# Optimization experiments

Hardware: AMD Instinct MI355X
Metric: run time of the kernel (lower is better)

## Reference

```python
import jax, jax.numpy as jnp
import numpy as np

WS = 7          # window size
NH = 12         # num heads
DIM = 384
HID = 4 * DIM
EPS = 1e-5


def _rel_pos_index(ws):
    coords = np.stack(np.meshgrid(np.arange(ws), np.arange(ws), indexing='ij'))  # (2,ws,ws)
    cf = coords.reshape(2, -1)
    rel = cf[:, :, None] - cf[:, None, :]           # (2,N,N)
    rel = rel.transpose(1, 2, 0)                    # (N,N,2)
    rel[:, :, 0] += ws - 1
    rel[:, :, 1] += ws - 1
    rel[:, :, 0] *= 2 * ws - 1
    return jnp.asarray(rel.sum(-1))                 # (N,N) int

REL_IDX = _rel_pos_index(WS)


def _layernorm(x, g, b):
    m = x.mean(-1, keepdims=True)
    v = ((x - m) ** 2).mean(-1, keepdims=True)
    return (x - m) * jax.lax.rsqrt(v + EPS) * g + b


def setup_inputs() -> dict:
    key = jax.random.key(0)
    ks = jax.random.split(key, 16)
    B, H, W = 8, 112, 112
    s = lambda fan: 1.0 / np.sqrt(fan)
    return {
        'x': jax.random.normal(ks[0], (B, DIM, H, W), jnp.float32),
        'g1': jnp.ones((DIM,), jnp.float32),
        'b1': jnp.zeros((DIM,), jnp.float32),
        'w_qkv': jax.random.normal(ks[1], (DIM, 3 * DIM), jnp.float32) * s(DIM),
        'b_qkv': jnp.zeros((3 * DIM,), jnp.float32),
        'rpb': jax.random.normal(ks[2], ((2 * WS - 1) ** 2, NH), jnp.float32) * 0.02,
        'w_proj': jax.random.normal(ks[3], (DIM, DIM), jnp.float32) * s(DIM),
        'b_proj': jnp.zeros((DIM,), jnp.float32),
        'g2': jnp.ones((DIM,), jnp.float32),
        'b2': jnp.zeros((DIM,), jnp.float32),
        'w_fc1': jax.random.normal(ks[4], (DIM, HID), jnp.float32) * s(DIM),
        'b_fc1': jnp.zeros((HID,), jnp.float32),
        'w_fc2': jax.random.normal(ks[5], (HID, DIM), jnp.float32) * s(HID),
        'b_fc2': jnp.zeros((DIM,), jnp.float32),
    }


def reference(x, g1, b1, w_qkv, b_qkv, rpb, w_proj, b_proj, g2, b2, w_fc1, b_fc1, w_fc2, b_fc2):
    B, C, H, W = x.shape
    x = x.transpose(0, 2, 3, 1)                     # (B,H,W,C)
    shortcut = x
    xn = _layernorm(x, g1, b1)

    # window partition (with padding, no-op when divisible)
    pad_h = (-H) % WS
    pad_w = (-W) % WS
    if pad_h or pad_w:
        xn = jnp.pad(xn, ((0, 0), (0, pad_h), (0, pad_w), (0, 0)))
    Hp, Wp = H + pad_h, W + pad_w
    N = WS * WS
    xw = xn.reshape(B, Hp // WS, WS, Wp // WS, WS, C).transpose(0, 1, 3, 2, 4, 5)
    xw = xw.reshape(-1, N, C)                       # (B_, N, C)
    B_ = xw.shape[0]
    hd = C // NH

    qkv = (xw @ w_qkv + b_qkv).reshape(B_, N, 3, NH, hd)
    q = qkv[:, :, 0].transpose(0, 2, 1, 3) * (hd ** -0.5)   # (B_,h,N,d)
    k = qkv[:, :, 1].transpose(0, 2, 1, 3)
    v = qkv[:, :, 2].transpose(0, 2, 1, 3)

    attn = jnp.einsum('bhnd,bhmd->bhnm', q, k)
    bias = rpb[REL_IDX.reshape(-1)].reshape(N, N, NH).transpose(2, 0, 1)  # (h,N,N)
    attn = jax.nn.softmax(attn + bias[None], axis=-1)

    out = jnp.einsum('bhnm,bhmd->bhnd', attn, v).transpose(0, 2, 1, 3).reshape(B_, N, C)
    out = out @ w_proj + b_proj

    # window reverse
    out = out.reshape(B, Hp // WS, Wp // WS, WS, WS, C).transpose(0, 1, 3, 2, 4, 5)
    out = out.reshape(B, Hp, Wp, C)[:, :H, :W]

    x = shortcut + out
    h = _layernorm(x, g2, b2)
    h = jax.nn.gelu(h @ w_fc1 + b_fc1, approximate=False) @ w_fc2 + b_fc2
    x = x + h
    return x.transpose(0, 3, 1, 2)                  # (B,C,H,W)
```

## Files before the change

kernel.cpp:

```cpp
#include <hip/hip_runtime.h>
#include <cstdint>
#include <cmath>

using u16 = unsigned short;

typedef __bf16 bf16x8 __attribute__((ext_vector_type(8)));
typedef float  f32x4  __attribute__((ext_vector_type(4)));

__device__ __forceinline__ float b2f(u16 u) {
    return __uint_as_float(((unsigned int)u) << 16);
}
__device__ __forceinline__ u16 f2b(float f) {
    unsigned int x = __float_as_uint(f);
    unsigned int r = (x + 0x7fffu + ((x >> 16) & 1u)) >> 16;
    return (u16)r;
}
__device__ __forceinline__ u16 f2b_fast(float f) {
    union { __bf16 h; u16 u; } cv;
    cv.h = (__bf16)f;
    return cv.u;
}

__device__ __forceinline__ void gload16(const u16* g, u16* l) {
    __builtin_amdgcn_global_load_lds((__attribute__((address_space(1))) void*)g,
                                     (__attribute__((address_space(3))) void*)l,
                                     16, 0, 0);
}

#define LGKM0_FENCE() do { \
    asm volatile("s_waitcnt lgkmcnt(0)" ::: "memory"); \
    __builtin_amdgcn_sched_barrier(0); } while (0)

__device__ __forceinline__ float gelu_f(float x) {
    float z = fabsf(x) * 0.70710678118f;
    float t = __builtin_amdgcn_rcpf(fmaf(0.3275911f, z, 1.0f));
    float poly = fmaf(fmaf(fmaf(fmaf(1.061405429f, t, -1.453152027f),
                               t, 1.421413741f),
                          t, -0.284496736f),
                     t, 0.254829592f) * t;
    float e = __expf(-z * z);
    float erfv = copysignf(1.0f - poly * e, x);
    return 0.5f * x * (1.0f + erfv);
}

__device__ __forceinline__ int tprime(int b, int hw) {
    int r = hw / 112, c = hw - r * 112;
    int wy = r / 7, iy = r - wy * 7;
    int wx = c / 7, ix = c - wx * 7;
    return (b * 256 + wy * 16 + wx) * 49 + iy * 7 + ix;
}

__global__ void detect_dtype(const unsigned int* __restrict__ x, int* __restrict__ flag) {
    __shared__ int cnt[256];
    int tid = threadIdx.x;
    int c = 0;
#pragma unroll
    for (int i = 0; i < 16; ++i) {
        unsigned int w = x[tid * 16 + i];
        int e = (w >> 23) & 0xFF;
        if (e >= 100 && e <= 150) ++c;
    }
    cnt[tid] = c;
    __syncthreads();
    if (tid == 0) {
        int s = 0;
        for (int i = 0; i < 256; ++i) s += cnt[i];
        flag[0] = (s > 3072) ? 1 : 0;
    }
}

__global__ void prep_small(const void* g1, const void* b1, const void* bqkv,
                           const void* bproj, const void* g2, const void* b2,
                           const void* bfc1, const void* bfc2, const void* rpb,
                           u16* cg1, u16* cb1, u16* cbqkv, u16* cbproj,
                           u16* cg2, u16* cb2, u16* cbfc1, u16* cbfc2,
                           float* bias_exp, const int* __restrict__ flagp) {
    int isf = flagp[0];
    int tid = threadIdx.x;
    auto cv = [&](const void* s, int i) {
        return isf ? f2b(((const float*)s)[i]) : ((const u16*)s)[i];
    };
    for (int i = tid; i < 384; i += 256) cg1[i] = cv(g1, i);
    for (int i = tid; i < 384; i += 256) cb1[i] = cv(b1, i);
    for (int i = tid; i < 1152; i += 256) cbqkv[i] = cv(bqkv, i);
    for (int i = tid; i < 384; i += 256) cbproj[i] = cv(bproj, i);
    for (int i = tid; i < 384; i += 256) cg2[i] = cv(g2, i);
    for (int i = tid; i < 384; i += 256) cb2[i] = cv(b2, i);
    for (int i = tid; i < 1536; i += 256) cbfc1[i] = cv(bfc1, i);
    for (int i = tid; i < 384; i += 256) cbfc2[i] = cv(bfc2, i);
    for (int i = tid; i < 12 * 64 * 64; i += 256) {
        int h = i >> 12, row = (i >> 6) & 63, col = i & 63;
        float v = -1e30f;
        if (row < 49 && col < 49) {
            int ri = row / 7, rj = row - ri * 7;
            int mi = col / 7, mj = col - mi * 7;
            int idx = ((ri - mi + 6) * 13 + (rj - mj + 6)) * 12 + h;
            v = isf ? ((const float*)rpb)[idx] : b2f(((const u16*)rpb)[idx]);
        }
        bias_exp[i] = v;
    }
}

__global__ void prep_w(const void* w0, const void* w1, const void* w2, const void* w3,
                       u16* o0, u16* o1, u16* o2, u16* o3,
                       const int* __restrict__ flagp) {
    __shared__ u16 tile[32][33];
    int isf = flagp[0];
    const void* src; u16* dst; int K, N;
    switch (blockIdx.z) {
        case 0: src = w0; dst = o0; K = 384;  N = 1152; break;
        case 1: src = w1; dst = o1; K = 384;  N = 384;  break;
        case 2: src = w2; dst = o2; K = 384;  N = 1536; break;
        default: src = w3; dst = o3; K = 1536; N = 384; break;
    }
    if ((int)blockIdx.x >= N / 32 || (int)blockIdx.y >= K / 32) return;
    int n0 = blockIdx.x * 32, k0 = blockIdx.y * 32;
    int tx = threadIdx.x & 31, ty = threadIdx.x >> 5;
#pragma unroll
    for (int i = 0; i < 4; ++i) {
        size_t idx = (size_t)(k0 + ty + i * 8) * N + n0 + tx;
        tile[ty + i * 8][tx] = isf ? f2b(((const float*)src)[idx])
                                   : ((const u16*)src)[idx];
    }
    __syncthreads();
#pragma unroll
    for (int i = 0; i < 4; ++i)
        dst[(size_t)(n0 + ty + i * 8) * K + k0 + tx] = tile[tx][ty + i * 8];
}

__global__ void ln1_fused(const void* __restrict__ x, const u16* __restrict__ g1,
                          const u16* __restrict__ b1, u16* __restrict__ xt,
                          u16* __restrict__ xn, const int* __restrict__ flagp) {
    __shared__ float tile[64][66];
    __shared__ float part[4][64];
    __shared__ float part2[4][64];
    __shared__ float stat[2][64];
    int isf = flagp[0];
    int hw0 = blockIdx.x * 64, b = blockIdx.y;
    int tid = threadIdx.x, hl = tid & 63, cq = tid >> 6;
    size_t base = (size_t)b * 384 * 12544 + hw0 + hl;
    float s = 0.f, sq = 0.f;
    for (int ci = 0; ci < 96; ++ci) {
        int c = cq * 96 + ci;
        float v = isf ? ((const float*)x)[base + (size_t)c * 12544]
                      : b2f(((const u16*)x)[base + (size_t)c * 12544]);
        s += v; sq += v * v;
    }
    part[cq][hl] = s;
    part2[cq][hl] = sq;
    __syncthreads();
    if (tid < 64) {
        float S1 = part[0][tid] + part[1][tid] + part[2][tid] + part[3][tid];
        float S2 = part2[0][tid] + part2[1][tid] + part2[2][tid] + part2[3][tid];
        float m = S1 * (1.0f / 384.0f);
        float var = S2 * (1.0f / 384.0f) - m * m;
        stat[0][tid] = m;
        stat[1][tid] = rsqrtf(var + 1e-5f);
    }
    __syncthreads();
    for (int ch = 0; ch < 6; ++ch) {
#pragma unroll
        for (int k = 0; k < 16; ++k) {
            int c = ch * 64 + cq * 16 + k;
            float v = isf ? ((const float*)x)[base + (size_t)c * 12544]
                          : b2f(((const u16*)x)[base + (size_t)c * 12544]);
            tile[cq * 16 + k][hl] = v;
        }
        __syncthreads();
#pragma unroll
        for (int k2 = 0; k2 < 16; ++k2) {
            int tok = cq * 16 + k2;
            int tp = tprime(b, hw0 + tok);
            float m = stat[0][tok], rs = stat[1][tok];
            int c = ch * 64 + hl;
            float v = tile[hl][tok];
            float g = b2f(g1[c]), bb = b2f(b1[c]);
            size_t o = (size_t)tp * 384 + c;
            xt[o] = f2b_fast(v);
            xn[o] = f2b_fast((v - m) * rs * g + bb);
        }
        __syncthreads();
    }
}

template <int EPI, int N, int K>
__global__ void gemm_bt(const u16* __restrict__ A, const u16* __restrict__ Bt,
                        const u16* __restrict__ bias, const u16* __restrict__ res,
                        u16* __restrict__ Cout, int M) {
    __shared__ __align__(16) u16 S[2][2][128 * 32];
    const int tid = threadIdx.x;
    const int wave = tid >> 6, lane = tid & 63;

    const int nbx = gridDim.x;
    const int nwg = nbx * gridDim.y;
    int flat = blockIdx.y * nbx + blockIdx.x;
    {
        int q = nwg >> 3, r = nwg & 7;
        int xcd = flat & 7, loc = flat >> 3;
        flat = (xcd < r ? xcd * (q + 1) : r * (q + 1) + (xcd - r) * q) + loc;
    }
    const int m0 = (flat / nbx) * 128, n0 = (flat % nbx) * 128;

    const int wm = wave & 1, wn = wave >> 1;
    const int m15 = lane & 15, q4 = lane >> 4;

    const u16* gA = A + (size_t)(m0 + wave * 32 + (lane >> 2)) * K + (lane & 3) * 8;
    const u16* gB = Bt + (size_t)(n0 + wave * 32 + (lane >> 2)) * K + (lane & 3) * 8;

    f32x4 acc[4][4];
#pragma unroll
    for (int i = 0; i < 4; ++i)
#pragma unroll
        for (int j = 0; j < 4; ++j) acc[i][j] = {0.f, 0.f, 0.f, 0.f};

    constexpr int nt = K >> 5;
    {
        u16* lA = &S[0][0][(wave * 32) * 32];
        u16* lB = &S[0][1][(wave * 32) * 32];
        gload16(gA, lA);
        gload16(gA + 16 * (size_t)K, lA + 16 * 32);
        gload16(gB, lB);
        gload16(gB + 16 * (size_t)K, lB + 16 * 32);
    }
    __syncthreads();

    for (int t = 0; t < nt; ++t) {
        const int cur = t & 1;
        if (t + 1 < nt) {
            const int k0 = (t + 1) << 5;
            u16* lA = &S[cur ^ 1][0][(wave * 32) * 32];
            u16* lB = &S[cur ^ 1][1][(wave * 32) * 32];
            gload16(gA + k0, lA);
            gload16(gA + k0 + 16 * (size_t)K, lA + 16 * 32);
            gload16(gB + k0, lB);
            gload16(gB + k0 + 16 * (size_t)K, lB + 16 * 32);
        }
        bf16x8 af[4], bfr[4];
#pragma unroll
        for (int i = 0; i < 4; ++i)
            af[i] = *(const bf16x8*)&S[cur][0][(wm * 64 + i * 16 + m15) * 32 + q4 * 8];
#pragma unroll
        for (int j = 0; j < 4; ++j)
            bfr[j] = *(const bf16x8*)&S[cur][1][(wn * 64 + j * 16 + m15) * 32 + q4 * 8];
#pragma unroll
        for (int i = 0; i < 4; ++i)
#pragma unroll
            for (int j = 0; j < 4; ++j)
                acc[i][j] = __builtin_amdgcn_mfma_f32_16x16x32_bf16(af[i], bfr[j],
                                                                    acc[i][j], 0, 0, 0);
        __syncthreads();
    }

    if (EPI <= 1) {
        u16* W = &S[0][0][0] + wave * 4096;
#pragma unroll
        for (int jj = 0; jj < 4; ++jj) {
            int n = n0 + wn * 64 + jj * 16 + m15;
            float bv = b2f(bias[n]);
#pragma unroll
            for (int i = 0; i < 4; ++i)
#pragma unroll
                for (int r = 0; r < 4; ++r) {
                    float v = acc[i][jj][r] + bv;
                    if (EPI == 1) v = gelu_f(v);
                    W[(i * 16 + q4 * 4 + r) * 64 + jj * 16 + m15] = f2b_fast(v);
                }
        }
#pragma unroll
        for (int o = 0; o < 8; ++o) {
            int lrow = o * 8 + (lane >> 3);
            int c8 = (lane & 7) * 8;
            uint4 v = *(const uint4*)&W[lrow * 64 + c8];
            *(uint4*)&Cout[(size_t)(m0 + wm * 64 + lrow) * N + n0 + wn * 64 + c8] = v;
        }
    } else {
        constexpr int CSTR = 132;
        float* Cs = (float*)&S[0][0][0];
#pragma unroll
        for (int p = 0; p < 4; ++p) {
            __syncthreads();
            if (wm == (p >> 1)) {
                const int ibase = (p & 1) * 2;
#pragma unroll
                for (int jj = 0; jj < 4; ++jj) {
                    int n = n0 + wn * 64 + jj * 16 + m15;
                    float bv = b2f(bias[n]);
#pragma unroll
                    for (int ii = 0; ii < 2; ++ii) {
                        int i = ibase + ii;
#pragma unroll
                        for (int r = 0; r < 4; ++r) {
                            float v = acc[i][jj][r] + bv;
                            Cs[(ii * 16 + q4 * 4 + r) * CSTR + wn * 64 + jj * 16 + m15] = v;
                        }
                    }
                }
            }
            __syncthreads();
#pragma unroll
            for (int it = 0; it < 2; ++it) {
                int r2 = it * 16 + (tid >> 4);
                int c8 = (tid & 15) * 8;
                size_t goff = (size_t)(m0 + p * 32 + r2) * N + n0 + c8;
                f32x4 v0 = *(const f32x4*)&Cs[r2 * CSTR + c8];
                f32x4 v1 = *(const f32x4*)&Cs[r2 * CSTR + c8 + 4];
                uint4 rv = *(const uint4*)&res[goff];
                const u16* rp = (const u16*)&rv;
                u16 outv[8];
#pragma unroll
                for (int e = 0; e < 4; ++e) {
                    outv[e] = f2b_fast(v0[e] + b2f(rp[e]));
                    outv[4 + e] = f2b_fast(v1[e] + b2f(rp[4 + e]));
                }
                *(uint4*)&Cout[goff] = *(const uint4*)outv;
            }
        }
    }
}

__global__ __launch_bounds__(256, 3)
void attn_win(const u16* __restrict__ qkv, const float* __restrict__ bias_exp,
              u16* __restrict__ outp) {
    __shared__ __align__(16) u16 lds[4][4096];
    const int tid = threadIdx.x;
    const int wave = tid >> 6, lane = tid & 63;
    const int t0p = blockIdx.x * 49;
    u16* Vt = &lds[wave][0];
    u16* Ps = &lds[wave][0];
    u16* Po = &lds[wave][0];
    const int m15 = lane & 15, q4 = lane >> 4;
    const int rr = lane >> 2, dq = lane & 3;
    const float scale = 0.17677669529663687f;
    const u16* wbase = qkv + (size_t)t0p * 1152;

    auto loadQK = [&](int h, bf16x8* qf, bf16x8* kf) {
#pragma unroll
        for (int i = 0; i < 4; ++i) {
            int row = i * 16 + m15;
            int rc = row < 49 ? row : 48;
            const u16* g = wbase + (size_t)rc * 1152 + h * 32 + q4 * 8;
            qf[i] = *(const bf16x8*)g;
            kf[i] = *(const bf16x8*)(g + 384);
        }
    };
    auto loadV = [&](int h, uint4* vv) {
#pragma unroll
        for (int p = 0; p < 4; ++p) {
            int n = p * 16 + rr;
            vv[p] = {0u, 0u, 0u, 0u};
            if (n < 49)
                vv[p] = *(const uint4*)(wbase + (size_t)n * 1152 + 768 + h * 32 + dq * 8);
        }
    };

    bf16x8 qfA[4], kfA[4];
    uint4 vvA[4];
    loadQK(wave, qfA, kfA);
    loadV(wave, vvA);

#pragma unroll
    for (int hl = 0; hl < 3; ++hl) {
        const int h = hl * 4 + wave;
#pragma unroll
        for (int p = 0; p < 4; ++p) {
            int n = p * 16 + rr;
            const u16* pv = (const u16*)&vvA[p];
#pragma unroll
            for (int ii = 0; ii < 8; ++ii) Vt[(dq * 8 + ii) * 64 + n] = pv[ii];
        }
        bf16x8 qfB[4], kfB[4];
        uint4 vvB[4];
        if (hl < 2) {
            loadQK(h + 4, qfB, kfB);
            loadV(h + 4, vvB);
        }
        LGKM0_FENCE();
        bf16x8 vf[2][2];
#pragma unroll
        for (int j = 0; j < 2; ++j)
#pragma unroll
            for (int kk = 0; kk < 2; ++kk)
                vf[j][kk] = *(const bf16x8*)&Vt[(j * 16 + m15) * 64 + kk * 32 + q4 * 8];
        f32x4 sc[4][4];
#pragma unroll
        for (int i = 0; i < 4; ++i)
#pragma unroll
            for (int j = 0; j < 4; ++j) {
                sc[i][j] = {0.f, 0.f, 0.f, 0.f};
                sc[i][j] = __builtin_amdgcn_mfma_f32_16x16x32_bf16(qfA[i], kfA[j],
                                                                   sc[i][j], 0, 0, 0);
            }
        const float* bx = bias_exp + h * 4096;
#pragma unroll
        for (int i = 0; i < 4; ++i)
#pragma unroll
            for (int r = 0; r < 4; ++r) {
                int row = i * 16 + q4 * 4 + r;
#pragma unroll
                for (int j = 0; j < 4; ++j)
                    sc[i][j][r] = fmaf(sc[i][j][r], scale, bx[row * 64 + j * 16 + m15]);
            }
#pragma unroll
        for (int i = 0; i < 4; ++i) {
#pragma unroll
            for (int r = 0; r < 4; ++r) {
                float mx = fmaxf(fmaxf(sc[i][0][r], sc[i][1][r]),
                                 fmaxf(sc[i][2][r], sc[i][3][r]));
                mx = fmaxf(mx, __shfl_xor(mx, 1));
                mx = fmaxf(mx, __shfl_xor(mx, 2));
                mx = fmaxf(mx, __shfl_xor(mx, 4));
                mx = fmaxf(mx, __shfl_xor(mx, 8));
                float e0 = __expf(sc[i][0][r] - mx);
                float e1 = __expf(sc[i][1][r] - mx);
                float e2 = __expf(sc[i][2][r] - mx);
                float e3 = __expf(sc[i][3][r] - mx);
                float sum = e0 + e1 + e2 + e3;
                sum += __shfl_xor(sum, 1);
                sum += __shfl_xor(sum, 2);
                sum += __shfl_xor(sum, 4);
                sum += __shfl_xor(sum, 8);
                float inv = 1.0f / sum;
                sc[i][0][r] = e0 * inv;
                sc[i][1][r] = e1 * inv;
                sc[i][2][r] = e2 * inv;
                sc[i][3][r] = e3 * inv;
            }
        }
#pragma unroll
        for (int i = 0; i < 4; ++i)
#pragma unroll
            for (int r = 0; r < 4; ++r)
#pragma unroll
                for (int j = 0; j < 4; ++j)
                    Ps[(i * 16 + q4 * 4 + r) * 64 + j * 16 + m15] = f2b(sc[i][j][r]);
        LGKM0_FENCE();
        f32x4 oacc[4][2];
#pragma unroll
        for (int i = 0; i < 4; ++i)
#pragma unroll
            for (int j = 0; j < 2; ++j) oacc[i][j] = {0.f, 0.f, 0.f, 0.f};
#pragma unroll
        for (int i = 0; i < 4; ++i) {
#pragma unroll
            for (int kk = 0; kk < 2; ++kk) {
                bf16x8 pf = *(const bf16x8*)&Ps[(i * 16 + m15) * 64 + kk * 32 + q4 * 8];
#pragma unroll
                for (int j = 0; j < 2; ++j)
                    oacc[i][j] = __builtin_amdgcn_mfma_f32_16x16x32_bf16(pf, vf[j][kk],
                                                                         oacc[i][j], 0, 0, 0);
            }
        }
#pragma unroll
        for (int i = 0; i < 4; ++i)
#pragma unroll
            for (int r = 0; r < 4; ++r) {
                int row = i * 16 + q4 * 4 + r;
#pragma unroll
                for (int j = 0; j < 2; ++j)
                    Po[row * 40 + j * 16 + m15] = f2b(oacc[i][j][r]);
            }
        LGKM0_FENCE();
#pragma unroll
        for (int w2 = 0; w2 < 4; ++w2) {
            int row = w2 * 16 + rr;
            if (row < 49) {
                uint4 ov = *(const uint4*)&Po[row * 40 + dq * 8];
                *(uint4*)&outp[(size_t)(t0p + row) * 384 + h * 32 + dq * 8] = ov;
            }
        }
        if (hl < 2) {
#pragma unroll
            for (int i = 0; i < 4; ++i) {
                qfA[i] = qfB[i];
                kfA[i] = kfB[i];
                vvA[i] = vvB[i];
            }
        }
    }
}

__global__ void ln2_kernel(const u16* __restrict__ y, const u16* __restrict__ g2,
                           const u16* __restrict__ b2, u16* __restrict__ out) {
    int wave = threadIdx.x >> 6, lane = threadIdx.x & 63;
    size_t t = (size_t)blockIdx.x * 4 + wave;
    uint3 rv = *(const uint3*)(y + t * 384 + lane * 6);
    float v[6];
    v[0] = b2f((u16)(rv.x & 0xffff)); v[1] = b2f((u16)(rv.x >> 16));
    v[2] = b2f((u16)(rv.y & 0xffff)); v[3] = b2f((u16)(rv.y >> 16));
    v[4] = b2f((u16)(rv.z & 0xffff)); v[5] = b2f((u16)(rv.z >> 16));
    float s = 0.f, sq = 0.f;
#pragma unroll
    for (int i = 0; i < 6; ++i) { s += v[i]; sq += v[i] * v[i]; }
#pragma unroll
    for (int m = 1; m < 64; m <<= 1) {
        s += __shfl_xor(s, m);
        sq += __shfl_xor(sq, m);
    }
    float mean = s * (1.0f / 384.0f);
    float var = sq * (1.0f / 384.0f) - mean * mean;
    float rstd = rsqrtf(var + 1e-5f);
    uint3 gv = *(const uint3*)(g2 + lane * 6);
    uint3 bv = *(const uint3*)(b2 + lane * 6);
    float g[6], bb[6];
    g[0] = b2f((u16)(gv.x & 0xffff)); g[1] = b2f((u16)(gv.x >> 16));
    g[2] = b2f((u16)(gv.y & 0xffff)); g[3] = b2f((u16)(gv.y >> 16));
    g[4] = b2f((u16)(gv.z & 0xffff)); g[5] = b2f((u16)(gv.z >> 16));
    bb[0] = b2f((u16)(bv.x & 0xffff)); bb[1] = b2f((u16)(bv.x >> 16));
    bb[2] = b2f((u16)(bv.y & 0xffff)); bb[3] = b2f((u16)(bv.y >> 16));
    bb[4] = b2f((u16)(bv.z & 0xffff)); bb[5] = b2f((u16)(bv.z >> 16));
    u16 o[6];
#pragma unroll
    for (int i = 0; i < 6; ++i)
        o[i] = f2b_fast((v[i] - mean) * rstd * g[i] + bb[i]);
    uint3 ov;
    ov.x = (unsigned)o[0] | ((unsigned)o[1] << 16);
    ov.y = (unsigned)o[2] | ((unsigned)o[3] << 16);
    ov.z = (unsigned)o[4] | ((unsigned)o[5] << 16);
    *(uint3*)(out + t * 384 + lane * 6) = ov;
}

__global__ void out_transpose(const u16* __restrict__ fin, void* __restrict__ out,
                              const int* __restrict__ flagp) {
    __shared__ float tile[64][65];
    int isf = flagp[0];
    int hw0 = blockIdx.x * 64, c0 = blockIdx.y * 64, b = blockIdx.z;
    int tid = threadIdx.x;
    {
        int cl = tid & 63, hq = tid >> 6;
#pragma unroll
        for (int it = 0; it < 16; ++it) {
            int hl = hq * 16 + it;
            int tp = tprime(b, hw0 + hl);
            tile[hl][cl] = b2f(fin[(size_t)tp * 384 + c0 + cl]);
        }
    }
    __syncthreads();
    {
        int hl = tid & 63, cq = tid >> 6;
#pragma unroll
        for (int it = 0; it < 16; ++it) {
            int cl = cq * 16 + it;
            size_t o = ((size_t)b * 384 + c0 + cl) * 12544 + hw0 + hl;
            float v = tile[hl][cl];
            if (isf) ((float*)out)[o] = v;
            else     ((u16*)out)[o] = f2b(v);
        }
    }
}

extern "C" void kernel_launch(void* const* d_in, const int* in_sizes, int n_in,
                              void* d_out, int out_size, void* d_ws, size_t ws_size,
                              hipStream_t stream) {
    constexpr int T = 100352, C = 384, HID = 1536, NQ = 1152;
    const void* x = d_in[0];

    char* ws = (char*)d_ws;
    size_t off = 0;
    auto alloc = [&](size_t bytes) { char* p = ws + off; off += (bytes + 255) & ~(size_t)255; return p; };
    int* flag = (int*)alloc(4);
    u16* cb_qkv  = (u16*)alloc((size_t)NQ * 2);
    u16* cb_proj = (u16*)alloc((size_t)C * 2);
    u16* cg1     = (u16*)alloc((size_t)C * 2);
    u16* cb1     = (u16*)alloc((size_t)C * 2);
    u16* cg2     = (u16*)alloc((size_t)C * 2);
    u16* cb2     = (u16*)alloc((size_t)C * 2);
    u16* cb_fc1  = (u16*)alloc((size_t)HID * 2);
    u16* cb_fc2  = (u16*)alloc((size_t)C * 2);
    u16* wqkvT  = (u16*)alloc((size_t)C * NQ * 2);
    u16* wprojT = (u16*)alloc((size_t)C * C * 2);
    u16* wfc1T  = (u16*)alloc((size_t)C * HID * 2);
    u16* wfc2T  = (u16*)alloc((size_t)HID * C * 2);
    float* biasx = (float*)alloc((size_t)12 * 64 * 64 * 4);
    u16* xt   = (u16*)alloc((size_t)T * C * 2);
    u16* bufB = (u16*)alloc((size_t)T * C * 2);
    u16* bufC = (u16*)alloc((size_t)T * HID * 2);
    u16* ybuf = (u16*)alloc((size_t)T * C * 2);

    detect_dtype<<<1, 256, 0, stream>>>((const unsigned int*)x, flag);

    prep_small<<<1, 256, 0, stream>>>(d_in[1], d_in[2], d_in[4], d_in[7], d_in[8],
                                      d_in[9], d_in[11], d_in[13], d_in[5],
                                      cg1, cb1, cb_qkv, cb_proj, cg2, cb2,
                                      cb_fc1, cb_fc2, biasx, flag);
    prep_w<<<dim3(48, 48, 4), 256, 0, stream>>>(d_in[3], d_in[6], d_in[10], d_in[12],
                                                wqkvT, wprojT, wfc1T, wfc2T, flag);

    ln1_fused<<<dim3(196, 8), 256, 0, stream>>>(x, cg1, cb1, xt, bufB, flag);

    gemm_bt<0, NQ, C><<<dim3(NQ / 128, T / 128), 256, 0, stream>>>(
        bufB, wqkvT, cb_qkv, nullptr, bufC, T);
    attn_win<<<2048, 256, 0, stream>>>(bufC, biasx, bufB);

    gemm_bt<2, C, C><<<dim3(C / 128, T / 128), 256, 0, stream>>>(
        bufB, wprojT, cb_proj, xt, ybuf, T);
    ln2_kernel<<<T / 4, 256, 0, stream>>>(ybuf, cg2, cb2, bufB);

    gemm_bt<1, HID, C><<<dim3(HID / 128, T / 128), 256, 0, stream>>>(
        bufB, wfc1T, cb_fc1, nullptr, bufC, T);
    gemm_bt<2, C, HID><<<dim3(C / 128, T / 128), 256, 0, stream>>>(
        bufC, wfc2T, cb_fc2, ybuf, bufB, T);
    out_transpose<<<dim3(196, 6, 8), 256, 0, stream>>>(bufB, d_out, flag);
}
```

Measured before the change: 1.259 ms.

## Split window attention across head-groups per block and transpose score layout

Each block now handles one window and one group of four heads, so the grid triples and the per-block three-head loop with register prefetch goes away. QK^T is computed transposed (K as A operand), which lets the bias load as a float4 and makes the softmax row reductions mostly in-register, needing only two cross-lane shuffles. LDS accesses for V^T and P use an XOR swizzle to cut bank conflicts, P is packed into 64-bit stores, and rounding uses the hardware bf16 convert. The cost is more blocks, each with less work, and no overlap of the next head's loads with current compute.

```diff
diff --git a/kernel.cpp b/kernel.cpp
--- a/kernel.cpp
+++ b/kernel.cpp
@@ -324,157 +324,137 @@
     __shared__ __align__(16) u16 lds[4][4096];
     const int tid = threadIdx.x;
     const int wave = tid >> 6, lane = tid & 63;
-    const int t0p = blockIdx.x * 49;
+    const int win = blockIdx.x / 3;
+    const int hp = blockIdx.x - win * 3;
+    const int h = hp * 4 + wave;
+    const int t0p = win * 49;
     u16* Vt = &lds[wave][0];
     u16* Ps = &lds[wave][0];
     u16* Po = &lds[wave][0];
     const int m15 = lane & 15, q4 = lane >> 4;
     const int rr = lane >> 2, dq = lane & 3;
+    const int swz = (m15 & 7) << 3;
     const float scale = 0.17677669529663687f;
     const u16* wbase = qkv + (size_t)t0p * 1152;
 
-    auto loadQK = [&](int h, bf16x8* qf, bf16x8* kf) {
+    bf16x8 qf[4], kf[4];
+#pragma unroll
+    for (int i = 0; i < 4; ++i) {
+        int row = i * 16 + m15;
+        int rc = row < 49 ? row : 48;
+        const u16* g = wbase + (size_t)rc * 1152 + h * 32 + q4 * 8;
+        qf[i] = *(const bf16x8*)g;
+        kf[i] = *(const bf16x8*)(g + 384);
+    }
+#pragma unroll
+    for (int p = 0; p < 4; ++p) {
+        int n = p * 16 + rr;
+        uint4 vv = {0u, 0u, 0u, 0u};
+        if (n < 49)
+            vv = *(const uint4*)(wbase + (size_t)n * 1152 + 768 + h * 32 + dq * 8);
+        const u16* pv = (const u16*)&vv;
+#pragma unroll
+        for (int ii = 0; ii < 8; ++ii)
+            Vt[((dq * 8 + ii) * 64 + n) ^ (ii << 3)] = pv[ii];
+    }
+    LGKM0_FENCE();
+    bf16x8 vf[2][2];
+#pragma unroll
+    for (int j = 0; j < 2; ++j)
+#pragma unroll
+        for (int kk = 0; kk < 2; ++kk)
+            vf[j][kk] = *(const bf16x8*)&Vt[((j * 16 + m15) * 64 + kk * 32 + q4 * 8) ^ swz];
+    f32x4 sc[4][4];
+#pragma unroll
+    for (int j = 0; j < 4; ++j)
 #pragma unroll
         for (int i = 0; i < 4; ++i) {
-            int row = i * 16 + m15;
-            int rc = row < 49 ? row : 48;
-            const u16* g = wbase + (size_t)rc * 1152 + h * 32 + q4 * 8;
-            qf[i] = *(const bf16x8*)g;
-            kf[i] = *(const bf16x8*)(g + 384);
-        }
-    };
-    auto loadV = [&](int h, uint4* vv) {
-#pragma unroll
-        for (int p = 0; p < 4; ++p) {
-            int n = p * 16 + rr;
-            vv[p] = {0u, 0u, 0u, 0u};
-            if (n < 49)
-                vv[p] = *(const uint4*)(wbase + (size_t)n * 1152 + 768 + h * 32 + dq * 8);
-        }
-    };
-
-    bf16x8 qfA[4], kfA[4];
-    uint4 vvA[4];
-    loadQK(wave, qfA, kfA);
-    loadV(wave, vvA);
-
-#pragma unroll
-    for (int hl = 0; hl < 3; ++hl) {
-        const int h = hl * 4 + wave;
-#pragma unroll
-        for (int p = 0; p < 4; ++p) {
-            int n = p * 16 + rr;
-            const u16* pv = (const u16*)&vvA[p];
-#pragma unroll
-            for (int ii = 0; ii < 8; ++ii) Vt[(dq * 8 + ii) * 64 + n] = pv[ii];
-        }
-        bf16x8 qfB[4], kfB[4];
-        uint4 vvB[4];
-        if (hl < 2) {
-            loadQK(h + 4, qfB, kfB);
-            loadV(h + 4, vvB);
-        }
-        LGKM0_FENCE();
-        bf16x8 vf[2][2];
-#pragma unroll
-        for (int j = 0; j < 2; ++j)
-#pragma unroll
-            for (int kk = 0; kk < 2; ++kk)
-                vf[j][kk] = *(const bf16x8*)&Vt[(j * 16 + m15) * 64 + kk * 32 + q4 * 8];
-        f32x4 sc[4][4];
-#pragma unroll
-        for (int i = 0; i < 4; ++i)
-#pragma unroll
-            for (int j = 0; j < 4; ++j) {
-                sc[i][j] = {0.f, 0.f, 0.f, 0.f};
-                sc[i][j] = __builtin_amdgcn_mfma_f32_16x16x32_bf16(qfA[i], kfA[j],
-                                                                   sc[i][j], 0, 0, 0);
+            sc[j][i] = {0.f, 0.f, 0.f, 0.f};
+            sc[j][i] = __builtin_amdgcn_mfma_f32_16x16x32_bf16(kf[j], qf[i],
+                                                               sc[j][i], 0, 0, 0);
+        }
+    const float* bx = bias_exp + h * 4096;
+#pragma unroll
+    for (int i = 0; i < 4; ++i) {
+        int qrow = i * 16 + m15;
+#pragma unroll
+        for (int j = 0; j < 4; ++j) {
+            f32x4 b4 = *(const f32x4*)&bx[qrow * 64 + j * 16 + q4 * 4];
+#pragma unroll
+            for (int r = 0; r < 4; ++r)
+                sc[j][i][r] = fmaf(sc[j][i][r], scale, b4[r]);
+        }
+    }
+#pragma unroll
+    for (int i = 0; i < 4; ++i) {
+        float mx = sc[0][i][0];
+#pragma unroll
+        for (int j = 0; j < 4; ++j)
+#pragma unroll
+            for (int r = 0; r < 4; ++r) mx = fmaxf(mx, sc[j][i][r]);
+        mx = fmaxf(mx, __shfl_xor(mx, 16));
+        mx = fmaxf(mx, __shfl_xor(mx, 32));
+        float sum = 0.f;
+#pragma unroll
+        for (int j = 0; j < 4; ++j)
+#pragma unroll
+            for (int r = 0; r < 4; ++r) {
+                float e = __expf(sc[j][i][r] - mx);
+                sc[j][i][r] = e;
+                sum += e;
             }
-        const float* bx = bias_exp + h * 4096;
-#pragma unroll
-        for (int i = 0; i < 4; ++i)
-#pragma unroll
-            for (int r = 0; r < 4; ++r) {
-                int row = i * 16 + q4 * 4 + r;
-#pragma unroll
-                for (int j = 0; j < 4; ++j)
-                    sc[i][j][r] = fmaf(sc[i][j][r], scale, bx[row * 64 + j * 16 + m15]);
-            }
-#pragma unroll
-        for (int i = 0; i < 4; ++i) {
-#pragma unroll
-            for (int r = 0; r < 4; ++r) {
-                float mx = fmaxf(fmaxf(sc[i][0][r], sc[i][1][r]),
-                                 fmaxf(sc[i][2][r], sc[i][3][r]));
-                mx = fmaxf(mx, __shfl_xor(mx, 1));
-                mx = fmaxf(mx, __shfl_xor(mx, 2));
-                mx = fmaxf(mx, __shfl_xor(mx, 4));
-                mx = fmaxf(mx, __shfl_xor(mx, 8));
-                float e0 = __expf(sc[i][0][r] - mx);
-                float e1 = __expf(sc[i][1][r] - mx);
-                float e2 = __expf(sc[i][2][r] - mx);
-                float e3 = __expf(sc[i][3][r] - mx);
-                float sum = e0 + e1 + e2 + e3;
-                sum += __shfl_xor(sum, 1);
-                sum += __shfl_xor(sum, 2);
-                sum += __shfl_xor(sum, 4);
-                sum += __shfl_xor(sum, 8);
-                float inv = 1.0f / sum;
-                sc[i][0][r] = e0 * inv;
-                sc[i][1][r] = e1 * inv;
-                sc[i][2][r] = e2 * inv;
-                sc[i][3][r] = e3 * inv;
-            }
-        }
-#pragma unroll
-        for (int i = 0; i < 4; ++i)
-#pragma unroll
-            for (int r = 0; r < 4; ++r)
-#pragma unroll
-                for (int j = 0; j < 4; ++j)
-                    Ps[(i * 16 + q4 * 4 + r) * 64 + j * 16 + m15] = f2b(sc[i][j][r]);
-        LGKM0_FENCE();
-        f32x4 oacc[4][2];
-#pragma unroll
-        for (int i = 0; i < 4; ++i)
-#pragma unroll
-            for (int j = 0; j < 2; ++j) oacc[i][j] = {0.f, 0.f, 0.f, 0.f};
-#pragma unroll
-        for (int i = 0; i < 4; ++i) {
-#pragma unroll
-            for (int kk = 0; kk < 2; ++kk) {
-                bf16x8 pf = *(const bf16x8*)&Ps[(i * 16 + m15) * 64 + kk * 32 + q4 * 8];
-#pragma unroll
-                for (int j = 0; j < 2; ++j)
-                    oacc[i][j] = __builtin_amdgcn_mfma_f32_16x16x32_bf16(pf, vf[j][kk],
-                                                                         oacc[i][j], 0, 0, 0);
-            }
-        }
-#pragma unroll
-        for (int i = 0; i < 4; ++i)
-#pragma unroll
-            for (int r = 0; r < 4; ++r) {
-                int row = i * 16 + q4 * 4 + r;
-#pragma unroll
-                for (int j = 0; j < 2; ++j)
-                    Po[row * 40 + j * 16 + m15] = f2b(oacc[i][j][r]);
-            }
-        LGKM0_FENCE();
-#pragma unroll
-        for (int w2 = 0; w2 < 4; ++w2) {
-            int row = w2 * 16 + rr;
-            if (row < 49) {
-                uint4 ov = *(const uint4*)&Po[row * 40 + dq * 8];
-                *(uint4*)&outp[(size_t)(t0p + row) * 384 + h * 32 + dq * 8] = ov;
-            }
-        }
-        if (hl < 2) {
-#pragma unroll
-            for (int i = 0; i < 4; ++i) {
-                qfA[i] = qfB[i];
-                kfA[i] = kfB[i];
-                vvA[i] = vvB[i];
-            }
+        sum += __shfl_xor(sum, 16);
+        sum += __shfl_xor(sum, 32);
+        float inv = 1.0f / sum;
+#pragma unroll
+        for (int j = 0; j < 4; ++j)
+#pragma unroll
+            for (int r = 0; r < 4; ++r) sc[j][i][r] *= inv;
+    }
+#pragma unroll
+    for (int i = 0; i < 4; ++i)
+#pragma unroll
+        for (int j = 0; j < 4; ++j) {
+            unsigned lo = (unsigned)f2b_fast(sc[j][i][0]) |
+                          ((unsigned)f2b_fast(sc[j][i][1]) << 16);
+            unsigned hi = (unsigned)f2b_fast(sc[j][i][2]) |
+                          ((unsigned)f2b_fast(sc[j][i][3]) << 16);
+            uint2 w; w.x = lo; w.y = hi;
+            *(uint2*)&Ps[((i * 16 + m15) * 64 + j * 16 + q4 * 4) ^ swz] = w;
+        }
+    LGKM0_FENCE();
+    f32x4 oacc[4][2];
+#pragma unroll
+    for (int i = 0; i < 4; ++i)
+#pragma unroll
+        for (int j = 0; j < 2; ++j) oacc[i][j] = {0.f, 0.f, 0.f, 0.f};
+#pragma unroll
+    for (int i = 0; i < 4; ++i) {
+#pragma unroll
+        for (int kk = 0; kk < 2; ++kk) {
+            bf16x8 pf = *(const bf16x8*)&Ps[((i * 16 + m15) * 64 + kk * 32 + q4 * 8) ^ swz];
+#pragma unroll
+            for (int j = 0; j < 2; ++j)
+                oacc[i][j] = __builtin_amdgcn_mfma_f32_16x16x32_bf16(pf, vf[j][kk],
+                                                                     oacc[i][j], 0, 0, 0);
+        }
+    }
+#pragma unroll
+    for (int i = 0; i < 4; ++i)
+#pragma unroll
+        for (int r = 0; r < 4; ++r) {
+            int row = i * 16 + q4 * 4 + r;
+#pragma unroll
+            for (int j = 0; j < 2; ++j)
+                Po[row * 40 + j * 16 + m15] = f2b_fast(oacc[i][j][r]);
+        }
+    LGKM0_FENCE();
+#pragma unroll
+    for (int w2 = 0; w2 < 4; ++w2) {
+        int row = w2 * 16 + rr;
+        if (row < 49) {
+            uint4 ov = *(const uint4*)&Po[row * 40 + dq * 8];
+            *(uint4*)&outp[(size_t)(t0p + row) * 384 + h * 32 + dq * 8] = ov;
         }
     }
 }
@@ -589,7 +569,7 @@
 
     gemm_bt<0, NQ, C><<<dim3(NQ / 128, T / 128), 256, 0, stream>>>(
         bufB, wqkvT, cb_qkv, nullptr, bufC, T);
-    attn_win<<<2048, 256, 0, stream>>>(bufC, biasx, bufB);
+    attn_win<<<6144, 256, 0, stream>>>(bufC, biasx, bufB);
 
     gemm_bt<2, C, C><<<dim3(C / 128, T / 128), 256, 0, stream>>>(
         bufB, wprojT, cb_proj, xt, ybuf, T);
```

After: 1.135 ms. 9.9% less time.
